# Kernel optimization log

Measured on AMD Instinct MI355X. Metric: run time of the kernel, lower is better.

Reference implementation:

```python
import jax, jax.numpy as jnp
import numpy as np

N_NODES = 100000
N_EDGES = 3200000
OUT_CH = 128
X_DIM = 128


def setup_inputs() -> dict:
    key = jax.random.key(0)
    k1, k2, k3, k4 = jax.random.split(key, 4)
    x = jax.random.normal(k1, (N_NODES, X_DIM), dtype=jnp.float32)
    edge_index = jax.random.randint(k2, (2, N_EDGES), 0, N_NODES, dtype=jnp.int64)
    # torch nn.Linear(num_nodes, out_channels): weight [out, N], bias [out]
    W_weight = jax.random.normal(k3, (OUT_CH, N_NODES), dtype=jnp.float32) * (1.0 / np.sqrt(N_NODES))
    W_bias = jax.random.normal(k4, (OUT_CH,), dtype=jnp.float32) * 0.01
    return {"x": x, "edge_index": edge_index, "W_weight": W_weight, "W_bias": W_bias}


def reference(x, edge_index, W_weight, W_bias):
    """LINK forward: logits = A @ W.T + b, A = sparse COO adjacency from edge_index.

    A[r, c] = 1 for each edge (r, c), so row r of the output is
    sum_{c in neighbors(r)} W.T[c] + b  -> gather + segment_sum (SpMM).
    """
    N = x.shape[0]
    row, col = edge_index[0], edge_index[1]
    Wt = W_weight.T  # [N, out]
    gathered = Wt[col]  # [E, out] irregular gather
    logits = jax.ops.segment_sum(gathered, row, num_segments=N) + W_bias  # [N, out]
    return logits
```

## Files before the change

kernel.cpp:

```cpp
#include <hip/hip_runtime.h>
#include <hip/hip_bf16.h>


#define NCHUNK 256
#define RPB 64
#define MAXBUCK 1600
#define CAP 3072
#define SCAN_CHUNK 256

__global__ __launch_bounds__(256) void quant_kernel(const float* __restrict__ W,
                                                    unsigned char* __restrict__ Wt8,
                                                    float* __restrict__ scales,
                                                    int N) {
    __shared__ float tile[128][33];
    __shared__ float pmax[8][32];
    __shared__ float sinv[32];
    int cx = threadIdx.x;
    int oy = threadIdx.y;
    int c = blockIdx.x * 32 + cx;
    for (int k = 0; k < 16; ++k) {
        int o = oy * 16 + k;
        tile[o][cx] = (c < N) ? W[(size_t)o * N + c] : 0.f;
    }
    __syncthreads();
    float m = 0.f;
    for (int k = 0; k < 16; ++k) m = fmaxf(m, fabsf(tile[oy * 16 + k][cx]));
    pmax[oy][cx] = m;
    __syncthreads();
    if (oy == 0) {
        float mm = pmax[0][cx];
        for (int q = 1; q < 8; ++q) mm = fmaxf(mm, pmax[q][cx]);
        if (c < N) scales[c] = mm / 127.f;
        sinv[cx] = (mm > 0.f) ? 127.f / mm : 0.f;
    }
    __syncthreads();
    if (c < N) {
        float si = sinv[cx];
        unsigned int w[4];
#pragma unroll
        for (int d = 0; d < 4; ++d) {
            unsigned int acc = 0;
#pragma unroll
            for (int b = 0; b < 4; ++b) {
                int o = oy * 16 + d * 4 + b;
                int qi = __float2int_rn(tile[o][cx] * si);
                acc |= ((unsigned int)(qi & 0xff)) << (8 * b);
            }
            w[d] = acc;
        }
        *(uint4*)(Wt8 + (size_t)c * 128 + oy * 16) =
            make_uint4(w[0], w[1], w[2], w[3]);
    }
}

__global__ __launch_bounds__(256) void p1_hist(const int* __restrict__ row,
                                               int E, int nbuck,
                                               int* __restrict__ hist) {
    __shared__ int lh[MAXBUCK];
    int b = blockIdx.x;
    for (int k = threadIdx.x; k < nbuck; k += blockDim.x) lh[k] = 0;
    __syncthreads();
    int ch = (E + NCHUNK - 1) / NCHUNK;
    int s = b * ch, e = min(E, s + ch);
    for (int i = s + threadIdx.x; i < e; i += blockDim.x)
        atomicAdd(&lh[row[i] >> 6], 1);
    __syncthreads();
    for (int k = threadIdx.x; k < nbuck; k += blockDim.x)
        hist[k * NCHUNK + b] = lh[k];
}

__global__ void scan_sums(const int* __restrict__ v, int* __restrict__ bsums,
                          int M) {
    __shared__ int s[SCAN_CHUNK];
    int i = blockIdx.x * SCAN_CHUNK + threadIdx.x;
    s[threadIdx.x] = (i < M) ? v[i] : 0;
    __syncthreads();
    for (int off = SCAN_CHUNK / 2; off > 0; off >>= 1) {
        if (threadIdx.x < off) s[threadIdx.x] += s[threadIdx.x + off];
        __syncthreads();
    }
    if (threadIdx.x == 0) bsums[blockIdx.x] = s[0];
}

__global__ __launch_bounds__(256) void scan_offsets_par(int* __restrict__ bsums,
                                                        int nb) {
    __shared__ int s[256];
    __shared__ int carry;
    if (threadIdx.x == 0) carry = 0;
    __syncthreads();
    for (int base = 0; base < nb; base += 256) {
        int i = base + threadIdx.x;
        int v = (i < nb) ? bsums[i] : 0;
        s[threadIdx.x] = v;
        __syncthreads();
        for (int off = 1; off < 256; off <<= 1) {
            int t = (threadIdx.x >= off) ? s[threadIdx.x - off] : 0;
            __syncthreads();
            s[threadIdx.x] += t;
            __syncthreads();
        }
        int incl = s[threadIdx.x];
        int c = carry;
        __syncthreads();
        if (threadIdx.x == 255) carry = c + incl;
        if (i < nb) bsums[i] = c + incl - v;
        __syncthreads();
    }
}

__global__ void scan_final(const int* __restrict__ v,
                           const int* __restrict__ bsums,
                           int* __restrict__ S, int M) {
    __shared__ int s[SCAN_CHUNK];
    int i = blockIdx.x * SCAN_CHUNK + threadIdx.x;
    int x = (i < M) ? v[i] : 0;
    s[threadIdx.x] = x;
    __syncthreads();
    for (int off = 1; off < SCAN_CHUNK; off <<= 1) {
        int t = (threadIdx.x >= off) ? s[threadIdx.x - off] : 0;
        __syncthreads();
        s[threadIdx.x] += t;
        __syncthreads();
    }
    if (i < M) S[i] = bsums[blockIdx.x] + s[threadIdx.x] - x;
}

__global__ __launch_bounds__(256) void p1_scatter(const int* __restrict__ row,
                                                  const int* __restrict__ col,
                                                  int E, int nbuck,
                                                  const int* __restrict__ S,
                                                  unsigned* __restrict__ packed) {
    __shared__ int lc[MAXBUCK];
    int b = blockIdx.x;
    for (int k = threadIdx.x; k < nbuck; k += blockDim.x)
        lc[k] = S[k * NCHUNK + b];
    __syncthreads();
    int ch = (E + NCHUNK - 1) / NCHUNK;
    int s = b * ch, e = min(E, s + ch);
    for (int i = s + threadIdx.x; i < e; i += blockDim.x) {
        int r = row[i], c = col[i];
        int p = atomicAdd(&lc[r >> 6], 1);
        packed[p] = ((unsigned)(r & 63) << 17) | (unsigned)c;
    }
}

__global__ __launch_bounds__(256) void spmm_fused(
    const unsigned* __restrict__ packed, const int* __restrict__ S,
    const unsigned char* __restrict__ Wt8, const float* __restrict__ scales,
    const float* __restrict__ bias, float* __restrict__ out, int E, int N,
    int nbuck) {
    __shared__ unsigned grouped[CAP];
    __shared__ int hist[RPB];
    __shared__ int rowstart[RPB + 1];
    __shared__ int cursor[RPB];
    int k = blockIdx.x;
    int start = S[k * NCHUNK];
    int end = (k + 1 < nbuck) ? S[(k + 1) * NCHUNK] : E;
    int cnt = end - start;
    if (cnt > CAP) cnt = CAP;
    if (threadIdx.x < RPB) hist[threadIdx.x] = 0;
    __syncthreads();
    for (int i = threadIdx.x; i < cnt; i += blockDim.x)
        atomicAdd(&hist[packed[start + i] >> 17], 1);
    __syncthreads();
    if (threadIdx.x == 0) {
        int acc = 0;
        for (int r = 0; r < RPB; ++r) { rowstart[r] = acc; acc += hist[r]; }
        rowstart[RPB] = acc;
    }
    __syncthreads();
    if (threadIdx.x < RPB) cursor[threadIdx.x] = rowstart[threadIdx.x];
    __syncthreads();
    for (int i = threadIdx.x; i < cnt; i += blockDim.x) {
        unsigned e2 = packed[start + i];
        int p = atomicAdd(&cursor[e2 >> 17], 1);
        grouped[p] = e2 & 0x1FFFFu;
    }
    __syncthreads();
    int wave = threadIdx.x >> 6, lane = threadIdx.x & 63;
    float2 bvec = *(const float2*)(bias + lane * 2);
    for (int r = wave; r < RPB; r += 4) {
        int gr = k * RPB + r;
        if (gr >= N) break;
        int js = rowstart[r], je = rowstart[r + 1];
        float ax = 0.f, ay = 0.f;
        int j = js;
        for (; j + 8 <= je; j += 8) {
            unsigned short u[8];
            float s[8];
#pragma unroll
            for (int t = 0; t < 8; ++t) {
                int c = grouped[j + t];
                u[t] = *(const unsigned short*)(Wt8 + (size_t)c * 128 + lane * 2);
                s[t] = scales[c];
            }
#pragma unroll
            for (int t = 0; t < 8; ++t) {
                int b0 = (int)(signed char)(u[t] & 0xff);
                int b1 = (int)(signed char)(u[t] >> 8);
                ax = fmaf(s[t], (float)b0, ax);
                ay = fmaf(s[t], (float)b1, ay);
            }
        }
        for (; j < je; ++j) {
            int c = grouped[j];
            unsigned short u =
                *(const unsigned short*)(Wt8 + (size_t)c * 128 + lane * 2);
            float s = scales[c];
            ax = fmaf(s, (float)(int)(signed char)(u & 0xff), ax);
            ay = fmaf(s, (float)(int)(signed char)(u >> 8), ay);
        }
        float2 res;
        res.x = ax + bvec.x;
        res.y = ay + bvec.y;
        *(float2*)(out + (size_t)gr * 128 + lane * 2) = res;
    }
}

extern "C" void kernel_launch(void* const* d_in, const int* in_sizes, int n_in,
                              void* d_out, int out_size, void* d_ws,
                              size_t ws_size, hipStream_t stream) {
    const int* edge = (const int*)d_in[1];
    const float* W = (const float*)d_in[2];
    const float* bias = (const float*)d_in[3];
    float* out = (float*)d_out;

    const int N = in_sizes[0] / 128;
    const int E = in_sizes[1] / 2;
    const int* row = edge;
    const int* col = edge + E;

    const int nbuck = (N + RPB - 1) / RPB;
    const int M = nbuck * NCHUNK;
    const int nb = (M + SCAN_CHUNK - 1) / SCAN_CHUNK;

    auto align16 = [](size_t v) { return (v + 15) & ~(size_t)15; };
    char* ws = (char*)d_ws;
    size_t off = 0;
    unsigned char* Wt8 = (unsigned char*)(ws + off);
    off = align16(off + (size_t)N * 128);
    float* scales = (float*)(ws + off);
    off = align16(off + (size_t)N * sizeof(float));
    unsigned* packed = (unsigned*)(ws + off);
    off = align16(off + (size_t)E * sizeof(unsigned));
    int* hist = (int*)(ws + off);
    off = align16(off + (size_t)M * sizeof(int));
    int* S = (int*)(ws + off);
    off = align16(off + (size_t)M * sizeof(int));
    int* bsums = (int*)(ws + off);
    off = align16(off + (size_t)nb * sizeof(int));

    {
        dim3 block(32, 8);
        dim3 grid((N + 31) / 32);
        quant_kernel<<<grid, block, 0, stream>>>(W, Wt8, scales, N);
    }
    p1_hist<<<NCHUNK, 256, 0, stream>>>(row, E, nbuck, hist);
    scan_sums<<<nb, SCAN_CHUNK, 0, stream>>>(hist, bsums, M);
    scan_offsets_par<<<1, 256, 0, stream>>>(bsums, nb);
    scan_final<<<nb, SCAN_CHUNK, 0, stream>>>(hist, bsums, S, M);
    p1_scatter<<<NCHUNK, 256, 0, stream>>>(row, col, E, nbuck, S, packed);
    spmm_fused<<<nbuck, 256, 0, stream>>>(packed, S, Wt8, scales, bias, out, E,
                                          N, nbuck);
}
```

Baseline: 182.0 us.

## Carry scales in packed edges and split rows across half-waves with 4-byte gathers

The column scale is now looked up once during the scatter phase and stored with the edge as a uint2, and the Wt8 row offset is pre-shifted, so the SpMM loop no longer does a separate global scale load. Int8 weights are stored with a +128 offset so decoding is a plain unsigned byte extract, and the offset is removed at the end with a single term scaled by the sum of scales. Each wave now splits a row's edges between two 32-lane halves, each lane reading 4 bytes, and the halves are combined with cross-lane shuffles. In exchange the packed buffer and shared staging double in size, and the scatter phase does extra random scale reads.

```diff
diff --git a/kernel.cpp b/kernel.cpp
--- a/kernel.cpp
+++ b/kernel.cpp
@@ -43,7 +43,7 @@
 #pragma unroll
             for (int b = 0; b < 4; ++b) {
                 int o = oy * 16 + d * 4 + b;
-                int qi = __float2int_rn(tile[o][cx] * si);
+                int qi = __float2int_rn(tile[o][cx] * si) + 128;
                 acc |= ((unsigned int)(qi & 0xff)) << (8 * b);
             }
             w[d] = acc;
@@ -127,9 +127,10 @@
 
 __global__ __launch_bounds__(256) void p1_scatter(const int* __restrict__ row,
                                                   const int* __restrict__ col,
+                                                  const float* __restrict__ scales,
                                                   int E, int nbuck,
                                                   const int* __restrict__ S,
-                                                  unsigned* __restrict__ packed) {
+                                                  uint2* __restrict__ packed) {
     __shared__ int lc[MAXBUCK];
     int b = blockIdx.x;
     for (int k = threadIdx.x; k < nbuck; k += blockDim.x)
@@ -139,18 +140,19 @@
     int s = b * ch, e = min(E, s + ch);
     for (int i = s + threadIdx.x; i < e; i += blockDim.x) {
         int r = row[i], c = col[i];
+        float sc = scales[c];
         int p = atomicAdd(&lc[r >> 6], 1);
-        packed[p] = ((unsigned)(r & 63) << 17) | (unsigned)c;
+        packed[p] = make_uint2(((unsigned)(r & 63) << 24) | ((unsigned)c << 7),
+                               __float_as_uint(sc));
     }
 }
 
 __global__ __launch_bounds__(256) void spmm_fused(
-    const unsigned* __restrict__ packed, const int* __restrict__ S,
-    const unsigned char* __restrict__ Wt8, const float* __restrict__ scales,
-    const float* __restrict__ bias, float* __restrict__ out, int E, int N,
-    int nbuck) {
-    __shared__ unsigned grouped[CAP];
-    __shared__ int hist[RPB];
+    const uint2* __restrict__ packed, const int* __restrict__ S,
+    const unsigned char* __restrict__ Wt8, const float* __restrict__ bias,
+    float* __restrict__ out, int E, int N, int nbuck) {
+    __shared__ uint2 g2[CAP];
+    __shared__ int rhist[RPB];
     __shared__ int rowstart[RPB + 1];
     __shared__ int cursor[RPB];
     int k = blockIdx.x;
@@ -158,62 +160,107 @@
     int end = (k + 1 < nbuck) ? S[(k + 1) * NCHUNK] : E;
     int cnt = end - start;
     if (cnt > CAP) cnt = CAP;
-    if (threadIdx.x < RPB) hist[threadIdx.x] = 0;
+    if (threadIdx.x < RPB) rhist[threadIdx.x] = 0;
     __syncthreads();
     for (int i = threadIdx.x; i < cnt; i += blockDim.x)
-        atomicAdd(&hist[packed[start + i] >> 17], 1);
+        atomicAdd(&rhist[packed[start + i].x >> 24], 1);
     __syncthreads();
     if (threadIdx.x == 0) {
         int acc = 0;
-        for (int r = 0; r < RPB; ++r) { rowstart[r] = acc; acc += hist[r]; }
+        for (int r = 0; r < RPB; ++r) { rowstart[r] = acc; acc += rhist[r]; }
         rowstart[RPB] = acc;
     }
     __syncthreads();
     if (threadIdx.x < RPB) cursor[threadIdx.x] = rowstart[threadIdx.x];
     __syncthreads();
     for (int i = threadIdx.x; i < cnt; i += blockDim.x) {
-        unsigned e2 = packed[start + i];
-        int p = atomicAdd(&cursor[e2 >> 17], 1);
-        grouped[p] = e2 & 0x1FFFFu;
-    }
-    __syncthreads();
+        uint2 e2 = packed[start + i];
+        int p = atomicAdd(&cursor[e2.x >> 24], 1);
+        g2[p] = make_uint2(e2.x & 0xFFFFFFu, e2.y);
+    }
+    __syncthreads();
+
     int wave = threadIdx.x >> 6, lane = threadIdx.x & 63;
-    float2 bvec = *(const float2*)(bias + lane * 2);
+    int h = lane >> 5;
+    int lane4 = (lane & 31) * 4;
+
     for (int r = wave; r < RPB; r += 4) {
         int gr = k * RPB + r;
         if (gr >= N) break;
         int js = rowstart[r], je = rowstart[r + 1];
-        float ax = 0.f, ay = 0.f;
-        int j = js;
-        for (; j + 8 <= je; j += 8) {
-            unsigned short u[8];
-            float s[8];
-#pragma unroll
-            for (int t = 0; t < 8; ++t) {
-                int c = grouped[j + t];
-                u[t] = *(const unsigned short*)(Wt8 + (size_t)c * 128 + lane * 2);
-                s[t] = scales[c];
-            }
-#pragma unroll
-            for (int t = 0; t < 8; ++t) {
-                int b0 = (int)(signed char)(u[t] & 0xff);
-                int b1 = (int)(signed char)(u[t] >> 8);
-                ax = fmaf(s[t], (float)b0, ax);
-                ay = fmaf(s[t], (float)b1, ay);
-            }
-        }
-        for (; j < je; ++j) {
-            int c = grouped[j];
-            unsigned short u =
-                *(const unsigned short*)(Wt8 + (size_t)c * 128 + lane * 2);
-            float s = scales[c];
-            ax = fmaf(s, (float)(int)(signed char)(u & 0xff), ax);
-            ay = fmaf(s, (float)(int)(signed char)(u >> 8), ay);
-        }
-        float2 res;
-        res.x = ax + bvec.x;
-        res.y = ay + bvec.y;
-        *(float2*)(out + (size_t)gr * 128 + lane * 2) = res;
+        int m = je - js;
+        int T = m >> 1;
+        float a0 = 0.f, a1 = 0.f, a2 = 0.f, a3 = 0.f, ss = 0.f;
+        int idx = js + h;
+        int t = 0;
+        for (; t + 4 <= T; t += 4) {
+            uint2 e0 = g2[idx + 0];
+            uint2 e1 = g2[idx + 2];
+            uint2 e2 = g2[idx + 4];
+            uint2 e3 = g2[idx + 6];
+            idx += 8;
+            uint32_t u0 = *(const uint32_t*)(Wt8 + (e0.x + lane4));
+            uint32_t u1 = *(const uint32_t*)(Wt8 + (e1.x + lane4));
+            uint32_t u2 = *(const uint32_t*)(Wt8 + (e2.x + lane4));
+            uint32_t u3 = *(const uint32_t*)(Wt8 + (e3.x + lane4));
+            float s0 = __uint_as_float(e0.y), s1 = __uint_as_float(e1.y);
+            float s2 = __uint_as_float(e2.y), s3 = __uint_as_float(e3.y);
+            a0 = fmaf(s0, (float)(u0 & 0xffu), a0);
+            a1 = fmaf(s0, (float)((u0 >> 8) & 0xffu), a1);
+            a2 = fmaf(s0, (float)((u0 >> 16) & 0xffu), a2);
+            a3 = fmaf(s0, (float)(u0 >> 24), a3);
+            ss += s0;
+            a0 = fmaf(s1, (float)(u1 & 0xffu), a0);
+            a1 = fmaf(s1, (float)((u1 >> 8) & 0xffu), a1);
+            a2 = fmaf(s1, (float)((u1 >> 16) & 0xffu), a2);
+            a3 = fmaf(s1, (float)(u1 >> 24), a3);
+            ss += s1;
+            a0 = fmaf(s2, (float)(u2 & 0xffu), a0);
+            a1 = fmaf(s2, (float)((u2 >> 8) & 0xffu), a1);
+            a2 = fmaf(s2, (float)((u2 >> 16) & 0xffu), a2);
+            a3 = fmaf(s2, (float)(u2 >> 24), a3);
+            ss += s2;
+            a0 = fmaf(s3, (float)(u3 & 0xffu), a0);
+            a1 = fmaf(s3, (float)((u3 >> 8) & 0xffu), a1);
+            a2 = fmaf(s3, (float)((u3 >> 16) & 0xffu), a2);
+            a3 = fmaf(s3, (float)(u3 >> 24), a3);
+            ss += s3;
+        }
+        for (; t < T; ++t) {
+            uint2 e0 = g2[idx];
+            idx += 2;
+            uint32_t u0 = *(const uint32_t*)(Wt8 + (e0.x + lane4));
+            float s0 = __uint_as_float(e0.y);
+            a0 = fmaf(s0, (float)(u0 & 0xffu), a0);
+            a1 = fmaf(s0, (float)((u0 >> 8) & 0xffu), a1);
+            a2 = fmaf(s0, (float)((u0 >> 16) & 0xffu), a2);
+            a3 = fmaf(s0, (float)(u0 >> 24), a3);
+            ss += s0;
+        }
+        if ((m & 1) && h == 0) {
+            uint2 e0 = g2[je - 1];
+            uint32_t u0 = *(const uint32_t*)(Wt8 + (e0.x + lane4));
+            float s0 = __uint_as_float(e0.y);
+            a0 = fmaf(s0, (float)(u0 & 0xffu), a0);
+            a1 = fmaf(s0, (float)((u0 >> 8) & 0xffu), a1);
+            a2 = fmaf(s0, (float)((u0 >> 16) & 0xffu), a2);
+            a3 = fmaf(s0, (float)(u0 >> 24), a3);
+            ss += s0;
+        }
+        a0 += __shfl_xor(a0, 32);
+        a1 += __shfl_xor(a1, 32);
+        a2 += __shfl_xor(a2, 32);
+        a3 += __shfl_xor(a3, 32);
+        ss += __shfl_xor(ss, 32);
+        if (h == 0) {
+            float4 b4 = *(const float4*)(bias + lane4);
+            float4 res;
+            res.x = fmaf(-128.f, ss, a0) + b4.x;
+            res.y = fmaf(-128.f, ss, a1) + b4.y;
+            res.z = fmaf(-128.f, ss, a2) + b4.z;
+            res.w = fmaf(-128.f, ss, a3) + b4.w;
+            *(float4*)(out + (size_t)gr * 128 + lane4) = res;
+        }
     }
 }
 
@@ -241,8 +288,8 @@
     off = align16(off + (size_t)N * 128);
     float* scales = (float*)(ws + off);
     off = align16(off + (size_t)N * sizeof(float));
-    unsigned* packed = (unsigned*)(ws + off);
-    off = align16(off + (size_t)E * sizeof(unsigned));
+    uint2* packed = (uint2*)(ws + off);
+    off = align16(off + (size_t)E * sizeof(uint2));
     int* hist = (int*)(ws + off);
     off = align16(off + (size_t)M * sizeof(int));
     int* S = (int*)(ws + off);
@@ -259,7 +306,8 @@
     scan_sums<<<nb, SCAN_CHUNK, 0, stream>>>(hist, bsums, M);
     scan_offsets_par<<<1, 256, 0, stream>>>(bsums, nb);
     scan_final<<<nb, SCAN_CHUNK, 0, stream>>>(hist, bsums, S, M);
-    p1_scatter<<<NCHUNK, 256, 0, stream>>>(row, col, E, nbuck, S, packed);
-    spmm_fused<<<nbuck, 256, 0, stream>>>(packed, S, Wt8, scales, bias, out, E,
-                                          N, nbuck);
-}
+    p1_scatter<<<NCHUNK, 256, 0, stream>>>(row, col, scales, E, nbuck, S,
+                                           packed);
+    spmm_fused<<<nbuck, 256, 0, stream>>>(packed, S, Wt8, bias, out, E, N,
+                                          nbuck);
+}
```

Measured after the change: 179.5 us. Within noise of the previous version (-1.4%).
